# Optimization experiments

Hardware: AMD Instinct MI355X
Metric: run time of the kernel (lower is better)

The kernel has to match this reference:

```python
import jax, jax.numpy as jnp
import numpy as np

N, E, D = 50000, 800000, 128   # nodes, edges, input feature dim
HEADS, HC = 8, 16
H = HEADS * HC                 # 128 hidden width after concat
G, OUT = 64, 16                # graphs in batch, output classes
EPS_BN = 1e-5


def _gat_conv(x, src, dst, edge_attr, W, att_src, att_dst, We, att_edge, b):
    """PyG GATConv (concat=True, negative_slope=0.2, add_self_loops=True,
    fill_value='mean' for edge_attr, dropout inactive in eval)."""
    n = x.shape[0]
    # self-loop edge attr = per-node mean of incoming edge attrs
    ones = jnp.ones((src.shape[0], 1), x.dtype)
    deg = jax.ops.segment_sum(ones, dst, num_segments=n)
    ea_mean = jax.ops.segment_sum(edge_attr, dst, num_segments=n) / jnp.maximum(deg, 1.0)
    loop = jnp.arange(n, dtype=src.dtype)
    src_f = jnp.concatenate([src, loop])
    dst_f = jnp.concatenate([dst, loop])
    ea = jnp.concatenate([edge_attr, ea_mean])          # [E+N, 1]
    h = (x @ W).reshape(n, HEADS, HC)                   # [N, heads, hc]
    a_src = jnp.sum(h * att_src, axis=-1)               # [N, heads]
    a_dst = jnp.sum(h * att_dst, axis=-1)               # [N, heads]
    he = (ea @ We).reshape(-1, HEADS, HC)               # [E+N, heads, hc]
    a_e = jnp.sum(he * att_edge, axis=-1)               # [E+N, heads]
    alpha = jax.nn.leaky_relu(a_src[src_f] + a_dst[dst_f] + a_e, 0.2)
    # segment softmax over destination nodes
    amax = jax.ops.segment_max(alpha, dst_f, num_segments=n)
    ex = jnp.exp(alpha - amax[dst_f])
    denom = jax.ops.segment_sum(ex, dst_f, num_segments=n)
    coef = ex / (denom[dst_f] + 1e-16)                  # [E+N, heads]
    out = jax.ops.segment_sum(h[src_f] * coef[..., None], dst_f, num_segments=n)
    return out.reshape(n, H) + b


def setup_inputs() -> dict:
    key = jax.random.key(0)
    k = lambda i: jax.random.fold_in(key, i)
    nrm = lambda i, shape, s=0.1: jax.random.normal(k(i), shape, dtype=jnp.float32) * s
    inp = {
        "x": jax.random.normal(k(0), (N, D), dtype=jnp.float32),
        "edge_index": jax.random.randint(k(1), (2, E), 0, N, dtype=jnp.int32),
        "edge_weights": jax.random.normal(k(2), (E, 1), dtype=jnp.float32),
        "batch": jnp.sort(jax.random.randint(k(3), (N,), 0, G, dtype=jnp.int32)),
        "bn_gamma": jnp.ones((D,), jnp.float32),
        "bn_beta": jnp.zeros((D,), jnp.float32),
        "bn_mean": nrm(4, (D,)),
        "bn_var": jax.random.uniform(k(5), (D,), dtype=jnp.float32) + 0.5,
    }
    ci = 10
    for li, ind in [(1, D), (2, H), (3, H)]:
        inp[f"W{li}"] = nrm(ci, (ind, H)); ci += 1
        inp[f"att_src{li}"] = nrm(ci, (HEADS, HC)); ci += 1
        inp[f"att_dst{li}"] = nrm(ci, (HEADS, HC)); ci += 1
        inp[f"We{li}"] = nrm(ci, (1, H)); ci += 1
        inp[f"att_edge{li}"] = nrm(ci, (HEADS, HC)); ci += 1
        inp[f"b{li}"] = jnp.zeros((H,), jnp.float32)
    inp["Wl1"] = nrm(40, (H, 2 * HC)); inp["bl1"] = jnp.zeros((2 * HC,), jnp.float32)
    inp["Wl2"] = nrm(41, (2 * HC, OUT)); inp["bl2"] = jnp.zeros((OUT,), jnp.float32)
    return inp


def reference(x, edge_index, edge_weights, batch,
              bn_gamma, bn_beta, bn_mean, bn_var,
              W1, att_src1, att_dst1, We1, att_edge1, b1,
              W2, att_src2, att_dst2, We2, att_edge2, b2,
              W3, att_src3, att_dst3, We3, att_edge3, b3,
              Wl1, bl1, Wl2, bl2):
    src, dst = edge_index[0], edge_index[1]
    # BatchNorm (eval mode, running stats)
    h = (x - bn_mean) / jnp.sqrt(bn_var + EPS_BN) * bn_gamma + bn_beta
    h = jax.nn.relu(_gat_conv(h, src, dst, edge_weights, W1, att_src1, att_dst1, We1, att_edge1, b1))
    h = jax.nn.relu(_gat_conv(h, src, dst, edge_weights, W2, att_src2, att_dst2, We2, att_edge2, b2))
    h = _gat_conv(h, src, dst, edge_weights, W3, att_src3, att_dst3, We3, att_edge3, b3)
    g = jax.ops.segment_max(h, batch, num_segments=G)   # global max pool -> [G, H]
    g = jax.nn.relu(g @ Wl1 + bl1)
    # dropout p=0.5 is identity in eval mode
    return g @ Wl2 + bl2
```

## Files before the change

### kernel.cpp

```cpp
#include <hip/hip_runtime.h>
#include <math.h>

#define NN 50000
#define NE 800000
#define NH 8
#define HDIM 128
#define NG 64
#define PSPLIT 16
#define MAXD 64

typedef __attribute__((ext_vector_type(8))) short bf16x8;
typedef __attribute__((ext_vector_type(4))) float f32x4;

static __device__ __forceinline__ float lrelu02(float x){ return x > 0.f ? x : 0.2f*x; }
static __device__ __forceinline__ unsigned short f2bf(float f){
    unsigned u = __float_as_uint(f);
    unsigned r = (u + 0x7FFFu + ((u >> 16) & 1u)) >> 16;
    return (unsigned short)r;
}
static __device__ __forceinline__ float bf2f(unsigned short h){ return __uint_as_float((unsigned)h << 16); }
static __device__ __forceinline__ float bf_lo(unsigned v){ return __uint_as_float(v << 16); }
static __device__ __forceinline__ float bf_hi(unsigned v){ return __uint_as_float(v & 0xFFFF0000u); }

__global__ void k_prep0(const float* W1, const float* W2, const float* W3,
                        unsigned short* Wth, unsigned short* Wtl,
                        const float* We1, const float* ae1, const float* We2, const float* ae2,
                        const float* We3, const float* ae3, float* wev,
                        const float* gam, const float* bet, const float* mean, const float* var,
                        float* sc, float* sh, unsigned* cnt){
    if (blockIdx.x >= 193){
        int i = (blockIdx.x - 193)*256 + threadIdx.x;
        if (i < NN) cnt[i] = 0;
        return;
    }
    if (blockIdx.x == 192){
        int t = threadIdx.x;
        if (t < 128){
            float s = gam[t] * rsqrtf(var[t] + 1e-5f);
            sc[t] = s; sh[t] = bet[t] - mean[t] * s;
        } else if (t < 152){
            int q = t - 128; int l = q >> 3, hd = q & 7;
            const float* We = (l == 0) ? We1 : (l == 1) ? We2 : We3;
            const float* ae = (l == 0) ? ae1 : (l == 1) ? ae2 : ae3;
            float s = 0.f;
            for (int c = 0; c < 16; c++) s += We[hd*16+c] * ae[hd*16+c];
            wev[q] = s;
        }
        return;
    }
    int i = blockIdx.x*256 + threadIdx.x;
    int l = i >> 14, rem = i & 16383;
    int k = rem >> 7, n = rem & 127;
    const float* W = (l==0) ? W1 : (l==1) ? W2 : W3;
    float w = W[k*128 + n];
    unsigned short hi = f2bf(w);
    unsigned short lo = f2bf(w - bf2f(hi));
    Wth[l*16384 + n*128 + k] = hi;
    Wtl[l*16384 + n*128 + k] = lo;
}

__global__ void k_scatter(const int* srcp, const int* dstp, const float* ew,
                          unsigned* cnt, unsigned* slab){
    int i = blockIdx.x*256 + threadIdx.x;
    if (i >= NE) return;
    int d = dstp[i];
    float w = ew[i];
    unsigned rank = atomicAdd(&cnt[d], 1u);
    if (rank < MAXD){
        unsigned ent = (unsigned)srcp[i] | ((unsigned)f2bf(w) << 16);
        __builtin_nontemporal_store(ent, &slab[(size_t)d*MAXD + rank]);
    }
}

__global__ __launch_bounds__(256, 3) void k_gemm1(const float* A,
        const unsigned short* Wth, const unsigned short* Wtl,
        const float* sc, const float* sh,
        const float* att_s, const float* att_d,
        unsigned* Hb, float* a_src, float* a_dst, int M){
    __shared__ unsigned short Ah[64][132];
    __shared__ unsigned short Al[64][132];
    int t = threadIdx.x;
    int row0 = blockIdx.x * 64;
    int w = t >> 6, l = t & 63;
    int lr = l & 15, lg = l >> 4;

    {
        const float2* A2 = (const float2*)A;
        for (int i = 0; i < 16; i++){
            int idx2 = t + i*256;
            int r = idx2 >> 6, c2 = idx2 & 63;
            float2 v = make_float2(0.f, 0.f);
            if (row0 + r < M){
                v = A2[(size_t)(row0+r)*64 + c2];
                float2 s2 = ((const float2*)sc)[c2], h2 = ((const float2*)sh)[c2];
                v.x = v.x*s2.x + h2.x; v.y = v.y*s2.y + h2.y;
            }
            unsigned short h0 = f2bf(v.x), h1 = f2bf(v.y);
            unsigned short l0 = f2bf(v.x - bf2f(h0)), l1 = f2bf(v.y - bf2f(h1));
            ((unsigned*)&Ah[r][0])[c2] = (unsigned)h0 | ((unsigned)h1 << 16);
            ((unsigned*)&Al[r][0])[c2] = (unsigned)l0 | ((unsigned)l1 << 16);
        }
    }
    __syncthreads();

    f32x4 acc[4][2];
    #pragma unroll
    for (int m = 0; m < 4; m++){ acc[m][0] = (f32x4){0,0,0,0}; acc[m][1] = (f32x4){0,0,0,0}; }

    #pragma unroll
    for (int ks = 0; ks < 4; ks++){
        int kk = ks*32 + lg*8;
        bf16x8 bh0 = *(const bf16x8*)&Wth[((w*2+0)*16 + lr)*128 + kk];
        bf16x8 bl0 = *(const bf16x8*)&Wtl[((w*2+0)*16 + lr)*128 + kk];
        bf16x8 bh1 = *(const bf16x8*)&Wth[((w*2+1)*16 + lr)*128 + kk];
        bf16x8 bl1 = *(const bf16x8*)&Wtl[((w*2+1)*16 + lr)*128 + kk];
        #pragma unroll
        for (int m = 0; m < 4; m++){
            bf16x8 a_h = *(const bf16x8*)&Ah[m*16 + lr][kk];
            bf16x8 a_l = *(const bf16x8*)&Al[m*16 + lr][kk];
            acc[m][0] = __builtin_amdgcn_mfma_f32_16x16x32_bf16(a_h, bh0, acc[m][0], 0, 0, 0);
            acc[m][0] = __builtin_amdgcn_mfma_f32_16x16x32_bf16(a_h, bl0, acc[m][0], 0, 0, 0);
            acc[m][0] = __builtin_amdgcn_mfma_f32_16x16x32_bf16(a_l, bh0, acc[m][0], 0, 0, 0);
            acc[m][1] = __builtin_amdgcn_mfma_f32_16x16x32_bf16(a_h, bh1, acc[m][1], 0, 0, 0);
            acc[m][1] = __builtin_amdgcn_mfma_f32_16x16x32_bf16(a_h, bl1, acc[m][1], 0, 0, 0);
            acc[m][1] = __builtin_amdgcn_mfma_f32_16x16x32_bf16(a_l, bh1, acc[m][1], 0, 0, 0);
        }
    }

    float asv[2], adv[2];
    #pragma unroll
    for (int n = 0; n < 2; n++){
        asv[n] = att_s[(w*2+n)*16 + lr];
        adv[n] = att_d[(w*2+n)*16 + lr];
    }
    #pragma unroll
    for (int m = 0; m < 4; m++){
        #pragma unroll
        for (int n = 0; n < 2; n++){
            #pragma unroll
            for (int r = 0; r < 4; r++){
                float v = acc[m][n][r];
                float pv = __shfl_xor(v, 1);
                int row = row0 + m*16 + lg*4 + r;
                if (!(l & 1) && row < M){
                    unsigned d = (unsigned)f2bf(v) | ((unsigned)f2bf(pv) << 16);
                    Hb[(size_t)row*64 + w*16 + n*8 + (lr >> 1)] = d;
                }
            }
        }
    }
    #pragma unroll
    for (int m = 0; m < 4; m++){
        #pragma unroll
        for (int r = 0; r < 4; r++){
            int row = row0 + m*16 + lg*4 + r;
            #pragma unroll
            for (int n = 0; n < 2; n++){
                float ps = acc[m][n][r] * asv[n];
                float pd = acc[m][n][r] * adv[n];
                #pragma unroll
                for (int off = 1; off < 16; off <<= 1){
                    ps += __shfl_xor(ps, off);
                    pd += __shfl_xor(pd, off);
                }
                if (lr == 0 && row < M){
                    a_src[row*NH + w*2 + n] = ps;
                    a_dst[row*NH + w*2 + n] = pd;
                }
            }
        }
    }
}

__global__ __launch_bounds__(256, 3) void k_gemm_bf(const unsigned* A16,
        const unsigned short* Wth, const unsigned short* Wtl,
        const float* att_s, const float* att_d,
        unsigned* Hb, float* a_src, float* a_dst, int M){
    __shared__ unsigned short Ah[64][132];
    int t = threadIdx.x;
    int row0 = blockIdx.x * 64;
    int w = t >> 6, l = t & 63;
    int lr = l & 15, lg = l >> 4;

    for (int i = 0; i < 16; i++){
        int idx = t + i*256;
        int r = idx >> 6, c2 = idx & 63;
        unsigned v = 0;
        if (row0 + r < M) v = A16[(size_t)(row0+r)*64 + c2];
        ((unsigned*)&Ah[r][0])[c2] = v;
    }
    __syncthreads();

    f32x4 acc[4][2];
    #pragma unroll
    for (int m = 0; m < 4; m++){ acc[m][0] = (f32x4){0,0,0,0}; acc[m][1] = (f32x4){0,0,0,0}; }

    #pragma unroll
    for (int ks = 0; ks < 4; ks++){
        int kk = ks*32 + lg*8;
        bf16x8 bh0 = *(const bf16x8*)&Wth[((w*2+0)*16 + lr)*128 + kk];
        bf16x8 bl0 = *(const bf16x8*)&Wtl[((w*2+0)*16 + lr)*128 + kk];
        bf16x8 bh1 = *(const bf16x8*)&Wth[((w*2+1)*16 + lr)*128 + kk];
        bf16x8 bl1 = *(const bf16x8*)&Wtl[((w*2+1)*16 + lr)*128 + kk];
        #pragma unroll
        for (int m = 0; m < 4; m++){
            bf16x8 a_h = *(const bf16x8*)&Ah[m*16 + lr][kk];
            acc[m][0] = __builtin_amdgcn_mfma_f32_16x16x32_bf16(a_h, bh0, acc[m][0], 0, 0, 0);
            acc[m][0] = __builtin_amdgcn_mfma_f32_16x16x32_bf16(a_h, bl0, acc[m][0], 0, 0, 0);
            acc[m][1] = __builtin_amdgcn_mfma_f32_16x16x32_bf16(a_h, bh1, acc[m][1], 0, 0, 0);
            acc[m][1] = __builtin_amdgcn_mfma_f32_16x16x32_bf16(a_h, bl1, acc[m][1], 0, 0, 0);
        }
    }

    float asv[2], adv[2];
    #pragma unroll
    for (int n = 0; n < 2; n++){
        asv[n] = att_s[(w*2+n)*16 + lr];
        adv[n] = att_d[(w*2+n)*16 + lr];
    }
    #pragma unroll
    for (int m = 0; m < 4; m++){
        #pragma unroll
        for (int n = 0; n < 2; n++){
            #pragma unroll
            for (int r = 0; r < 4; r++){
                float v = acc[m][n][r];
                float pv = __shfl_xor(v, 1);
                int row = row0 + m*16 + lg*4 + r;
                if (!(l & 1) && row < M){
                    unsigned d = (unsigned)f2bf(v) | ((unsigned)f2bf(pv) << 16);
                    Hb[(size_t)row*64 + w*16 + n*8 + (lr >> 1)] = d;
                }
            }
        }
    }
    #pragma unroll
    for (int m = 0; m < 4; m++){
        #pragma unroll
        for (int r = 0; r < 4; r++){
            int row = row0 + m*16 + lg*4 + r;
            #pragma unroll
            for (int n = 0; n < 2; n++){
                float ps = acc[m][n][r] * asv[n];
                float pd = acc[m][n][r] * adv[n];
                #pragma unroll
                for (int off = 1; off < 16; off <<= 1){
                    ps += __shfl_xor(ps, off);
                    pd += __shfl_xor(pd, off);
                }
                if (lr == 0 && row < M){
                    a_src[row*NH + w*2 + n] = ps;
                    a_dst[row*NH + w*2 + n] = pd;
                }
            }
        }
    }
}

__global__ __launch_bounds__(256) void k_aggr(const unsigned* cnt, const unsigned* slab,
                       const float* a_src, const float* a_dst, const float* wev,
                       const unsigned* Hb, const float* bias, unsigned* Out16, int do_relu){
    int wid = threadIdx.x >> 6, lane = threadIdx.x & 63;
    int n = blockIdx.x*4 + wid;
    if (n >= NN) return;
    unsigned dgt = cnt[n];
    int dg = (int)(dgt < MAXD ? dgt : MAXD);
    int hd = lane >> 3;
    int slot = lane >> 3;
    int headA = lane & 7;
    float adA = a_dst[n*NH + headA];
    float whA = wev[headA];
    unsigned vself = Hb[(size_t)n*64 + lane];
    float asnA = a_src[n*NH + headA];
    float accL0=0.f, accH0=0.f, accL1=0.f, accH1=0.f, den0=0.f, den1=0.f;
    float easumA = 0.f;
    const unsigned* srow = &slab[(size_t)n*MAXD];
    const uint4* srow4 = (const uint4*)srow;
    for (int base = 0; base < dg; base += 16){
        uint4 e0 = srow4[(base>>2)+0], e1 = srow4[(base>>2)+1];
        uint4 e2 = srow4[(base>>2)+2], e3 = srow4[(base>>2)+3];
        unsigned ent[16] = {e0.x,e0.y,e0.z,e0.w, e1.x,e1.y,e1.z,e1.w,
                            e2.x,e2.y,e2.z,e2.w, e3.x,e3.y,e3.z,e3.w};
        unsigned v[16];
        #pragma unroll
        for (int j = 0; j < 16; j++) v[j] = Hb[(size_t)(ent[j] & 0xFFFFu)*64 + lane];
        unsigned eA0 = srow[base + slot];
        unsigned eA1 = srow[base + 8 + slot];
        float ea0 = bf2f((unsigned short)(eA0 >> 16));
        float ea1 = bf2f((unsigned short)(eA1 >> 16));
        float as0 = a_src[(eA0 & 0xFFFFu)*NH + headA];
        float as1 = a_src[(eA1 & 0xFFFFu)*NH + headA];
        bool l0 = (base + slot) < dg, l1 = (base + 8 + slot) < dg;
        float c0 = l0 ? __expf(lrelu02(as0 + adA + ea0*whA)) : 0.f;
        float c1 = l1 ? __expf(lrelu02(as1 + adA + ea1*whA)) : 0.f;
        easumA += (l0 ? ea0 : 0.f) + (l1 ? ea1 : 0.f);
        #pragma unroll
        for (int j = 0; j < 8; j++){
            float cj = __shfl(c0, j*8 + hd);
            if (j & 1){ den1 += cj; accL1 += cj*bf_lo(v[j]); accH1 += cj*bf_hi(v[j]); }
            else      { den0 += cj; accL0 += cj*bf_lo(v[j]); accH0 += cj*bf_hi(v[j]); }
        }
        #pragma unroll
        for (int j = 0; j < 8; j++){
            float cj = __shfl(c1, j*8 + hd);
            if (j & 1){ den1 += cj; accL1 += cj*bf_lo(v[8+j]); accH1 += cj*bf_hi(v[8+j]); }
            else      { den0 += cj; accL0 += cj*bf_lo(v[8+j]); accH0 += cj*bf_hi(v[8+j]); }
        }
    }
    easumA += __shfl_xor(easumA, 8);
    easumA += __shfl_xor(easumA, 16);
    easumA += __shfl_xor(easumA, 32);
    float ea_self = easumA / fmaxf((float)dgt, 1.f);
    float csA = __expf(lrelu02(asnA + adA + ea_self*whA));
    float cs = __shfl(csA, hd);
    den0 += cs; accL0 += cs*bf_lo(vself); accH0 += cs*bf_hi(vself);
    float inv = 1.f / (den0 + den1 + 1e-16f);
    float2 bv = ((const float2*)bias)[lane];
    float o0 = (accL0 + accL1) * inv + bv.x;
    float o1 = (accH0 + accH1) * inv + bv.y;
    if (do_relu){ o0 = fmaxf(o0, 0.f); o1 = fmaxf(o1, 0.f); }
    Out16[(size_t)n*64 + lane] = (unsigned)f2bf(o0) | ((unsigned)f2bf(o1) << 16);
}

static __device__ int lower_bound_batch(const int* b, int v){
    int lo = 0, hi = NN;
    while (lo < hi){
        int mid = (lo + hi) >> 1;
        if (b[mid] < v) lo = mid + 1; else hi = mid;
    }
    return lo;
}

__global__ void k_pool1(const unsigned* A16, const int* batch, float* gpart){
    int g = blockIdx.x >> 4, s = blockIdx.x & (PSPLIT-1);
    int start = lower_bound_batch(batch, g);
    int end   = lower_bound_batch(batch, g + 1);
    int nrows = end - start;
    int chunk = (nrows + PSPLIT - 1) / PSPLIT;
    int rs = start + s*chunk;
    int re = rs + chunk; if (re > end) re = end;
    int c = threadIdx.x;
    float m0 = -INFINITY, m1 = -INFINITY;
    for (int r = rs; r < re; r++){
        unsigned v = A16[(size_t)r*64 + c];
        m0 = fmaxf(m0, bf_lo(v));
        m1 = fmaxf(m1, bf_hi(v));
    }
    ((float2*)&gpart[(size_t)blockIdx.x*HDIM])[c] = make_float2(m0, m1);
}

__global__ __launch_bounds__(256) void k_mlp(const float* gpart, const float* Wl1, const float* bl1,
                      const float* Wl2, const float* bl2, float* out){
    __shared__ float gl[NG*HDIM];
    __shared__ float t1[NG*32];
    int t = threadIdx.x;
    for (int i = 0; i < 32; i++){
        int o = t + i*256;
        int g = o >> 7, col = o & 127;
        float m = -INFINITY;
        for (int s = 0; s < PSPLIT; s++)
            m = fmaxf(m, gpart[(size_t)(g*PSPLIT+s)*HDIM + col]);
        gl[o] = m;
    }
    __syncthreads();
    for (int i = 0; i < 8; i++){
        int o = t + i*256;
        int gi = o >> 5, j = o & 31;
        float s = bl1[j];
        for (int k = 0; k < 128; k++) s += gl[gi*128 + k] * Wl1[k*32 + j];
        t1[o] = fmaxf(s, 0.f);
    }
    __syncthreads();
    for (int i = 0; i < 4; i++){
        int o = t + i*256;
        int gi = o >> 4, j = o & 15;
        float s = bl2[j];
        for (int k = 0; k < 32; k++) s += t1[gi*32 + k] * Wl2[k*16 + j];
        out[o] = s;
    }
}

extern "C" void kernel_launch(void* const* d_in, const int* in_sizes, int n_in,
                              void* d_out, int out_size, void* d_ws, size_t ws_size,
                              hipStream_t stream){
    const float* x    = (const float*)d_in[0];
    const int*   ei   = (const int*)d_in[1];
    const float* ew   = (const float*)d_in[2];
    const int*   batch= (const int*)d_in[3];
    const float* bng  = (const float*)d_in[4];
    const float* bnb  = (const float*)d_in[5];
    const float* bnm  = (const float*)d_in[6];
    const float* bnv  = (const float*)d_in[7];
    const float* Wmat[3] = {(const float*)d_in[8],  (const float*)d_in[14], (const float*)d_in[20]};
    const float* asr[3]  = {(const float*)d_in[9],  (const float*)d_in[15], (const float*)d_in[21]};
    const float* adt[3]  = {(const float*)d_in[10], (const float*)d_in[16], (const float*)d_in[22]};
    const float* Wep[3]  = {(const float*)d_in[11], (const float*)d_in[17], (const float*)d_in[23]};
    const float* aep[3]  = {(const float*)d_in[12], (const float*)d_in[18], (const float*)d_in[24]};
    const float* bp[3]   = {(const float*)d_in[13], (const float*)d_in[19], (const float*)d_in[25]};
    const float* Wl1 = (const float*)d_in[26];
    const float* bl1 = (const float*)d_in[27];
    const float* Wl2 = (const float*)d_in[28];
    const float* bl2 = (const float*)d_in[29];

    char* p = (char*)d_ws;
    auto alloc = [&](size_t bytes)->char*{
        char* r = p; p += (bytes + 255) & ~(size_t)255; return r;
    };
    unsigned* Hb    = (unsigned*)alloc((size_t)NN*64*4);
    unsigned* A16   = (unsigned*)alloc((size_t)NN*64*4);
    float*    a_src = (float*)alloc((size_t)NN*NH*4);
    float*    a_dst = (float*)alloc((size_t)NN*NH*4);
    unsigned* cnt   = (unsigned*)alloc((size_t)NN*4);
    unsigned* slab  = (unsigned*)alloc((size_t)NN*MAXD*4);
    float*    wev   = (float*)alloc(24*4);
    float*    scv   = (float*)alloc(128*4);
    float*    shv   = (float*)alloc(128*4);
    unsigned short* Wth = (unsigned short*)alloc((size_t)3*16384*2);
    unsigned short* Wtl = (unsigned short*)alloc((size_t)3*16384*2);
    float*    gpart = (float*)alloc((size_t)NG*PSPLIT*HDIM*4);

    const int* srcp = ei;
    const int* dstp = ei + NE;

    k_prep0<<<193 + 196, 256, 0, stream>>>(Wmat[0], Wmat[1], Wmat[2], Wth, Wtl,
                                     Wep[0], aep[0], Wep[1], aep[1], Wep[2], aep[2], wev,
                                     bng, bnb, bnm, bnv, scv, shv, cnt);
    k_scatter<<<(NE+255)/256, 256, 0, stream>>>(srcp, dstp, ew, cnt, slab);

    k_gemm1<<<(NN+63)/64, 256, 0, stream>>>(x, Wth, Wtl, scv, shv,
                                            asr[0], adt[0], Hb, a_src, a_dst, NN);
    k_aggr<<<(NN+3)/4, 256, 0, stream>>>(cnt, slab, a_src, a_dst, wev,
                                         Hb, bp[0], A16, 1);
    for (int l = 1; l < 3; l++){
        k_gemm_bf<<<(NN+63)/64, 256, 0, stream>>>(A16, Wth + l*16384, Wtl + l*16384,
                                                  asr[l], adt[l], Hb, a_src, a_dst, NN);
        k_aggr<<<(NN+3)/4, 256, 0, stream>>>(cnt, slab, a_src, a_dst, wev + l*8,
                                             Hb, bp[l], A16, (l < 2) ? 1 : 0);
    }
    k_pool1<<<NG*PSPLIT, 64, 0, stream>>>(A16, batch, gpart);
    k_mlp<<<1, 256, 0, stream>>>(gpart, Wl1, bl1, Wl2, bl2, (float*)d_out);
}
```

Baseline: 313.4 us.

## Fuse weight prep into scatter and partition edge scatter by destination residue

Merges the weight/BN prep kernel into the edge-scatter kernel and replaces the in-kernel counter zeroing with a memset. Each edge chunk is now processed by 8 blocks, and each block only inserts edges whose destination mod 8 matches its index. The intent is to localize atomics and slab writes per block and to save a kernel launch. The cost is that every edge's indices are read 8 times, and the nontemporal store becomes a normal store.

After: 301.3 us. 3.9% less time.

```diff
diff --git a/kernel.cpp b/kernel.cpp
--- a/kernel.cpp
+++ b/kernel.cpp
@@ -8,6 +8,8 @@
 #define NG 64
 #define PSPLIT 16
 #define MAXD 64
+#define SCATCH 3125
+#define SCATB (SCATCH*8)
 
 typedef __attribute__((ext_vector_type(8))) short bf16x8;
 typedef __attribute__((ext_vector_type(4))) float f32x4;
@@ -22,53 +24,54 @@
 static __device__ __forceinline__ float bf_lo(unsigned v){ return __uint_as_float(v << 16); }
 static __device__ __forceinline__ float bf_hi(unsigned v){ return __uint_as_float(v & 0xFFFF0000u); }
 
-__global__ void k_prep0(const float* W1, const float* W2, const float* W3,
-                        unsigned short* Wth, unsigned short* Wtl,
-                        const float* We1, const float* ae1, const float* We2, const float* ae2,
-                        const float* We3, const float* ae3, float* wev,
-                        const float* gam, const float* bet, const float* mean, const float* var,
-                        float* sc, float* sh, unsigned* cnt){
-    if (blockIdx.x >= 193){
-        int i = (blockIdx.x - 193)*256 + threadIdx.x;
-        if (i < NN) cnt[i] = 0;
+__global__ void k_scatter(const int* srcp, const int* dstp, const float* ew,
+                          unsigned* cnt, unsigned* slab,
+                          const float* W1, const float* W2, const float* W3,
+                          unsigned short* Wth, unsigned short* Wtl,
+                          const float* We1, const float* ae1, const float* We2, const float* ae2,
+                          const float* We3, const float* ae3, float* wev,
+                          const float* gam, const float* bet, const float* mean, const float* var,
+                          float* sc, float* sh){
+    int b = blockIdx.x;
+    if (b >= SCATB){
+        int pb = b - SCATB;
+        if (pb == 192){
+            int t = threadIdx.x;
+            if (t < 128){
+                float s = gam[t] * rsqrtf(var[t] + 1e-5f);
+                sc[t] = s; sh[t] = bet[t] - mean[t] * s;
+            } else if (t < 152){
+                int q = t - 128; int l = q >> 3, hd = q & 7;
+                const float* We = (l == 0) ? We1 : (l == 1) ? We2 : We3;
+                const float* ae = (l == 0) ? ae1 : (l == 1) ? ae2 : ae3;
+                float s = 0.f;
+                for (int c = 0; c < 16; c++) s += We[hd*16+c] * ae[hd*16+c];
+                wev[q] = s;
+            }
+            return;
+        }
+        int i = pb*256 + threadIdx.x;
+        int l = i >> 14, rem = i & 16383;
+        int k = rem >> 7, n = rem & 127;
+        const float* W = (l==0) ? W1 : (l==1) ? W2 : W3;
+        float w = W[k*128 + n];
+        unsigned short hi = f2bf(w);
+        unsigned short lo = f2bf(w - bf2f(hi));
+        Wth[l*16384 + n*128 + k] = hi;
+        Wtl[l*16384 + n*128 + k] = lo;
         return;
     }
-    if (blockIdx.x == 192){
-        int t = threadIdx.x;
-        if (t < 128){
-            float s = gam[t] * rsqrtf(var[t] + 1e-5f);
-            sc[t] = s; sh[t] = bet[t] - mean[t] * s;
-        } else if (t < 152){
-            int q = t - 128; int l = q >> 3, hd = q & 7;
-            const float* We = (l == 0) ? We1 : (l == 1) ? We2 : We3;
-            const float* ae = (l == 0) ? ae1 : (l == 1) ? ae2 : ae3;
-            float s = 0.f;
-            for (int c = 0; c < 16; c++) s += We[hd*16+c] * ae[hd*16+c];
-            wev[q] = s;
-        }
-        return;
-    }
-    int i = blockIdx.x*256 + threadIdx.x;
-    int l = i >> 14, rem = i & 16383;
-    int k = rem >> 7, n = rem & 127;
-    const float* W = (l==0) ? W1 : (l==1) ? W2 : W3;
-    float w = W[k*128 + n];
-    unsigned short hi = f2bf(w);
-    unsigned short lo = f2bf(w - bf2f(hi));
-    Wth[l*16384 + n*128 + k] = hi;
-    Wtl[l*16384 + n*128 + k] = lo;
-}
-
-__global__ void k_scatter(const int* srcp, const int* dstp, const float* ew,
-                          unsigned* cnt, unsigned* slab){
-    int i = blockIdx.x*256 + threadIdx.x;
+    int chunk = b >> 3, x = b & 7;
+    int i = chunk*256 + threadIdx.x;
     if (i >= NE) return;
-    int d = dstp[i];
+    int   d = dstp[i];
     float w = ew[i];
+    int   s = srcp[i];
+    if ((d & 7) != x) return;
     unsigned rank = atomicAdd(&cnt[d], 1u);
     if (rank < MAXD){
-        unsigned ent = (unsigned)srcp[i] | ((unsigned)f2bf(w) << 16);
-        __builtin_nontemporal_store(ent, &slab[(size_t)d*MAXD + rank]);
+        unsigned ent = (unsigned)s | ((unsigned)f2bf(w) << 16);
+        slab[(size_t)d*MAXD + rank] = ent;
     }
 }
 
@@ -422,10 +425,11 @@
     const int* srcp = ei;
     const int* dstp = ei + NE;
 
-    k_prep0<<<193 + 196, 256, 0, stream>>>(Wmat[0], Wmat[1], Wmat[2], Wth, Wtl,
+    hipMemsetAsync(cnt, 0, (size_t)NN*4, stream);
+    k_scatter<<<SCATB + 193, 256, 0, stream>>>(srcp, dstp, ew, cnt, slab,
+                                     Wmat[0], Wmat[1], Wmat[2], Wth, Wtl,
                                      Wep[0], aep[0], Wep[1], aep[1], Wep[2], aep[2], wev,
-                                     bng, bnb, bnm, bnv, scv, shv, cnt);
-    k_scatter<<<(NE+255)/256, 256, 0, stream>>>(srcp, dstp, ew, cnt, slab);
+                                     bng, bnb, bnm, bnv, scv, shv);
 
     k_gemm1<<<(NN+63)/64, 256, 0, stream>>>(x, Wth, Wtl, scv, shv,
                                             asr[0], adt[0], Hb, a_src, a_dst, NN);
```
